# Optimization experiments

Measured on AMD Instinct MI355X. Metric: run time of the kernel, lower is better.

The kernel has to match this reference:

```python
import jax, jax.numpy as jnp
import numpy as np

B, S, D = 32, 512, 1024
H, HD = 16, 64          # num_heads, head_dim
K = 64                  # downsampling_k
NEG = -9e15             # -9000000000000000.0 in source


def setup_inputs() -> dict:
    key0 = jax.random.key(0)
    ks = jax.random.split(key0, 8)
    glorot = lambda k, shape, fan: jax.random.uniform(k, shape, jnp.float32,
                                                      -np.sqrt(6.0 / fan), np.sqrt(6.0 / fan))
    fan = D + H * HD  # glorot_uniform over (hidden, heads*head_dim)
    return {
        "query": jax.random.normal(ks[0], (B, S, D), jnp.float32),
        "key": jax.random.normal(ks[1], (B, S, D), jnp.float32),
        "value": jax.random.normal(ks[2], (B, S, D), jnp.float32),
        "query_kernel": glorot(ks[3], (D, H, HD), fan),
        "key_kernel": glorot(ks[4], (D, H, HD), fan),
        "value_kernel": glorot(ks[5], (D, H, HD), fan),
        "key_downsample_mat": (1.0 / K) * jax.random.normal(ks[6], (K, S), jnp.float32),
        "value_downsample_mat": (1.0 / K) * jax.random.normal(ks[7], (K, S), jnp.float32),
    }


def reference(query, key, value, query_kernel, key_kernel, value_kernel,
              key_downsample_mat, value_downsample_mat):
    # Linformer-style downsampling of K/V along the sequence axis: [B,S,D] -> [B,K,D]
    key_ds = jnp.einsum('ks,bsd->bkd', key_downsample_mat, key)
    val_ds = jnp.einsum('ks,bsd->bkd', value_downsample_mat, value)

    # Per-head projections
    q = jnp.einsum('bsd,dnh->bsnh', query, query_kernel)   # [B,S,H,HD]
    k = jnp.einsum('bkd,dnh->bknh', key_ds, key_kernel)    # [B,K,H,HD]
    v = jnp.einsum('bkd,dnh->bknh', val_ds, value_kernel)  # [B,K,H,HD]

    # Masked softmax attention over the downsampled key set
    scores = jnp.einsum('bqnh,bknh->bnqk', q, k)           # [B,H,S,K]
    # Source builds tril over [S, K_down] then slices first K cols (no-op here)
    mask = jnp.tril(jnp.ones((S, K), dtype=bool))          # [S,K], broadcasts over B,H
    scores = jnp.where(mask, scores, NEG)
    attn = jax.nn.softmax(scores, axis=-1)                 # dropout deterministic (train=False)

    a_v = jnp.einsum('bnqk,bknh->bqnh', attn, v)           # [B,S,H,HD]
    return a_v.reshape(B, S, H * HD)
```

## Files before the change

kernel.cpp:

```cpp
#include <hip/hip_runtime.h>
#include <stdint.h>

#define B_   32
#define S_   512
#define D_   1024
#define H_   16
#define HD_  64
#define KD_  64
#define NH_  1024

typedef __attribute__((ext_vector_type(8))) short short8;
typedef __attribute__((ext_vector_type(4))) float floatx4;

#define GAS __attribute__((address_space(1)))
#define LAS __attribute__((address_space(3)))

__device__ __forceinline__ ushort f2bf(float f) {
  uint32_t u = __float_as_uint(f);
  u = u + 0x7FFFu + ((u >> 16) & 1u);
  return (ushort)(u >> 16);
}

__device__ __forceinline__ float bf2f(ushort h) {
  return __uint_as_float(((uint32_t)h) << 16);
}

__device__ __forceinline__ void gload_lds16(const void* g, void* l) {
  __builtin_amdgcn_global_load_lds((const GAS uint32_t*)g, (LAS uint32_t*)l, 16, 0, 0);
}

#define BARRIER() asm volatile("s_barrier" ::: "memory")
#define WAITLGKM() asm volatile("s_waitcnt lgkmcnt(0)" ::: "memory")

__global__ __launch_bounds__(256) void cvt_split(const float* __restrict__ kdm,
                                                 const float* __restrict__ vdm,
                                                 ushort* __restrict__ hi,
                                                 ushort* __restrict__ lo) {
  int i = blockIdx.x * 256 + threadIdx.x;
  const float* src = (i < 8192) ? kdm : vdm;
  int j = i & 8191;
  float4 v = ((const float4*)src)[j];
  ushort4 h, l;
  h.x = f2bf(v.x); l.x = f2bf(v.x - bf2f(h.x));
  h.y = f2bf(v.y); l.y = f2bf(v.y - bf2f(h.y));
  h.z = f2bf(v.z); l.z = f2bf(v.z - bf2f(h.z));
  h.w = f2bf(v.w); l.w = f2bf(v.w - bf2f(h.w));
  ((ushort4*)hi)[i] = h;
  ((ushort4*)lo)[i] = l;
}

__global__ __launch_bounds__(256, 6) void pre_kv(
    const float* __restrict__ key, const float* __restrict__ value,
    const float* __restrict__ kkm, const float* __restrict__ vkm,
    const ushort* __restrict__ dsm_hi, const ushort* __restrict__ dsm_lo,
    ushort* __restrict__ kkT, ushort* __restrict__ vkT,
    ushort* __restrict__ outk, ushort* __restrict__ outv) {
  __shared__ __align__(16) char smem[17408];
  const int blk = blockIdx.x;
  const int tid = threadIdx.x;

  if (blk < 1024) {
    const int bz = (blk & 7) + ((blk >> 7) << 3);
    const int t  = (blk >> 3) & 15;
    const int z = bz >> 5, b = bz & 31;
    const int c0 = t * 64;
    const float* in = z ? value : key;
    ushort* out     = z ? outv : outk;
    const ushort* Ah = dsm_hi + (size_t)z * (KD_ * S_);
    const ushort* Al = dsm_lo + (size_t)z * (KD_ * S_);

    ushort* lAh = (ushort*)smem;
    ushort* lAl = (ushort*)(smem + 4096);
    uint*   lBh = (uint*)(smem + 8192);
    uint*   lBl = (uint*)(smem + 12800);

    const int lane = tid & 63, w = tid >> 6;
    const int lr = lane & 15, lg = lane >> 4;
    const int wn = w * 16;
    const int lam = tid & 15;
    const int d0 = lam * 4;
    const int sp = tid >> 4;
    const int swz = lam & 12;

    floatx4 acc[4];
#pragma unroll
    for (int m = 0; m < 4; ++m) acc[m] = (floatx4){0.f, 0.f, 0.f, 0.f};

    const float* pbase = in + (size_t)b * S_ * D_ + c0 + d0;
    float4 ra = *(const float4*)(pbase + (size_t)(sp * 2) * D_);
    float4 rb = *(const float4*)(pbase + (size_t)(sp * 2 + 1) * D_);

    for (int k0 = 0; k0 < S_; k0 += 32) {
      {
        size_t src = (size_t)(tid >> 2) * S_ + k0 + (size_t)(tid & 3) * 8;
        gload_lds16(Ah + src, lAh + w * 512);
        gload_lds16(Al + src, lAl + w * 512);
      }
      {
        int col = sp ^ swz;
        const float* pa = (const float*)&ra;
        const float* pb = (const float*)&rb;
#pragma unroll
        for (int i = 0; i < 4; ++i) {
          ushort h0 = f2bf(pa[i]);
          ushort l0 = f2bf(pa[i] - bf2f(h0));
          ushort h1 = f2bf(pb[i]);
          ushort l1 = f2bf(pb[i] - bf2f(h1));
          lBh[(d0 + i) * 18 + col] = (uint)h0 | ((uint)h1 << 16);
          lBl[(d0 + i) * 18 + col] = (uint)l0 | ((uint)l1 << 16);
        }
      }
      if (k0 + 32 < S_) {
        const float* pn = pbase + (size_t)(k0 + 32) * D_;
        ra = *(const float4*)(pn + (size_t)(sp * 2) * D_);
        rb = *(const float4*)(pn + (size_t)(sp * 2 + 1) * D_);
        asm volatile("s_waitcnt vmcnt(2)" ::: "memory");
      } else {
        asm volatile("s_waitcnt vmcnt(0)" ::: "memory");
      }
      WAITLGKM();
      BARRIER();
      short8 bh, bl;
      {
        int d = wn + lr;
        int off = d * 18 + ((lg * 4) ^ ((d >> 2) & 12));
        bh = *(const short8*)&lBh[off];
        bl = *(const short8*)&lBl[off];
      }
#pragma unroll
      for (int m = 0; m < 4; ++m) {
        int aoff = (m * 16 + lr) * 32 + lg * 8;
        short8 ah = *(const short8*)&lAh[aoff];
        short8 al = *(const short8*)&lAl[aoff];
        acc[m] = __builtin_amdgcn_mfma_f32_16x16x32_bf16(ah, bh, acc[m], 0, 0, 0);
        acc[m] = __builtin_amdgcn_mfma_f32_16x16x32_bf16(ah, bl, acc[m], 0, 0, 0);
        acc[m] = __builtin_amdgcn_mfma_f32_16x16x32_bf16(al, bh, acc[m], 0, 0, 0);
      }
      BARRIER();
    }
    size_t obase = (size_t)b * KD_ * D_;
#pragma unroll
    for (int m = 0; m < 4; ++m)
#pragma unroll
      for (int r = 0; r < 4; ++r)
        out[obase + (size_t)(m * 16 + lg * 4 + r) * D_ + c0 + wn + lr] =
            f2bf(acc[m][r]);

  } else {
    const int blk2 = blk - 1024;
    const int tz = blk2 >> 10;
    const int rem = blk2 & 1023;
    const int tyb = rem >> 5;
    const int txb = rem & 31;
    const float* in = tz == 0 ? kkm : vkm;
    ushort* outp    = tz == 0 ? kkT : vkT;
    float (*tile)[33] = (float(*)[33])smem;
    const int tx = tid & 31, ty = tid >> 5;
    int x = txb * 32 + tx;
    int y0 = tyb * 32;
#pragma unroll
    for (int j = 0; j < 4; ++j)
      tile[ty + j * 8][tx] = in[(size_t)(y0 + ty + j * 8) * 1024 + x];
    __syncthreads();
    int x2 = tyb * 32 + tx;
    int y2 = txb * 32;
#pragma unroll
    for (int j = 0; j < 4; ++j)
      outp[(size_t)(y2 + ty + j * 8) * 1024 + x2] = f2bf(tile[tx][ty + j * 8]);
  }
}

__global__ __launch_bounds__(256) void gemm_kv_q(
    const ushort* __restrict__ A,
    const ushort* __restrict__ Bt,
    const ushort* __restrict__ Bt2,
    ushort* __restrict__ C,
    ushort* __restrict__ vpT,
    const float* __restrict__ qk, ushort* __restrict__ qkT,
    const float* __restrict__ query, ushort* __restrict__ q_bf) {
  __shared__ __align__(16) char smem[16384];
  const int blk = blockIdx.x;
  const int tid = threadIdx.x;

  if (blk < 256) {
    ushort* lA = (ushort*)smem;
    ushort* lB = (ushort*)(smem + 8192);
    int xcd = blk & 7, slot = blk >> 3;
    int mt = xcd * 4 + (slot >> 3);
    int nt = slot & 7;
    int m0 = mt * 128, n0 = nt * 128;
    const ushort* Bsel = (mt >= 16) ? Bt2 : Bt;

    int lane = tid & 63, w = tid >> 6;
    int lr = lane & 15, lg = lane >> 4;
    int wm = (w >> 1) * 64, wn = (w & 1) * 64;
    floatx4 acc[4][4];
#pragma unroll
    for (int m = 0; m < 4; ++m)
#pragma unroll
      for (int n = 0; n < 4; ++n) acc[m][n] = (floatx4){0.f, 0.f, 0.f, 0.f};

    for (int k0 = 0; k0 < 1024; k0 += 32) {
#pragma unroll
      for (int i = 0; i < 2; ++i) {
        int c = i * 256 + w * 64 + lane;
        gload_lds16(A + ((size_t)(m0 + (c >> 2)) * 1024 + k0 + (c & 3) * 8),
                    &lA[(i * 256 + w * 64) * 8]);
        gload_lds16(Bsel + ((size_t)(n0 + (c >> 2)) * 1024 + k0 + (c & 3) * 8),
                    &lB[(i * 256 + w * 64) * 8]);
      }
      __syncthreads();
      short8 af[4], bfr[4];
#pragma unroll
      for (int m = 0; m < 4; ++m)
        af[m] = *(const short8*)&lA[(wm + m * 16 + lr) * 32 + lg * 8];
#pragma unroll
      for (int n = 0; n < 4; ++n)
        bfr[n] = *(const short8*)&lB[(wn + n * 16 + lr) * 32 + lg * 8];
#pragma unroll
      for (int m = 0; m < 4; ++m)
#pragma unroll
        for (int n = 0; n < 4; ++n)
          acc[m][n] = __builtin_amdgcn_mfma_f32_16x16x32_bf16(af[m], bfr[n], acc[m][n], 0, 0, 0);
      __syncthreads();
    }
    if (mt < 16) {
#pragma unroll
      for (int m = 0; m < 4; ++m)
#pragma unroll
        for (int n = 0; n < 4; ++n)
#pragma unroll
          for (int r = 0; r < 4; ++r)
            C[(size_t)(m0 + wm + m * 16 + lg * 4 + r) * 1024 + n0 + wn + n * 16 + lr] =
                f2bf(acc[m][n][r]);
    } else {
#pragma unroll
      for (int m = 0; m < 4; ++m)
#pragma unroll
        for (int n = 0; n < 4; ++n) {
          int rowV = m0 - 2048 + wm + m * 16 + lg * 4;
          int b = rowV >> 6, k = rowV & 63;
          int hd = n0 + wn + n * 16 + lr;
          ushort4 o;
          o.x = f2bf(acc[m][n][0]); o.y = f2bf(acc[m][n][1]);
          o.z = f2bf(acc[m][n][2]); o.w = f2bf(acc[m][n][3]);
          *(ushort4*)&vpT[(size_t)b * 65536 + (size_t)hd * 64 + k] = o;
        }
    }

  } else if (blk < 256 + 1024) {
    const int blk2 = blk - 256;
    const int tyb = blk2 >> 5;
    const int txb = blk2 & 31;
    float (*tile)[33] = (float(*)[33])smem;
    const int tx = tid & 31, ty = tid >> 5;
    int x = txb * 32 + tx;
    int y0 = tyb * 32;
#pragma unroll
    for (int j = 0; j < 4; ++j)
      tile[ty + j * 8][tx] = qk[(size_t)(y0 + ty + j * 8) * 1024 + x];
    __syncthreads();
    int x2 = tyb * 32 + tx;
    int y2 = txb * 32;
#pragma unroll
    for (int j = 0; j < 4; ++j)
      qkT[(size_t)(y2 + ty + j * 8) * 1024 + x2] = f2bf(tile[tx][ty + j * 8]);

  } else {
    const size_t base = (size_t)(blk - 1280) * 2048 + tid;
#pragma unroll
    for (int j = 0; j < 8; ++j) {
      size_t i = base + (size_t)j * 256;
      float4 v = ((const float4*)query)[i];
      ushort4 o;
      o.x = f2bf(v.x); o.y = f2bf(v.y); o.z = f2bf(v.z); o.w = f2bf(v.w);
      ((ushort4*)q_bf)[i] = o;
    }
  }
}

__global__ __launch_bounds__(512, 2) void gemm256_attn(
    const ushort* __restrict__ A, const ushort* __restrict__ Bt,
    const ushort* __restrict__ kp, const ushort* __restrict__ vpT,
    float* __restrict__ out) {
  extern __shared__ ushort lds[];
  ushort* ldsA = lds;
  ushort* ldsB = lds + 2 * 256 * 64;
  const int tid = threadIdx.x;
  const int w = tid >> 6, lane = tid & 63;
  const int lr = lane & 15, lg = lane >> 4;
  const int wm = w >> 2, wn = w & 3;
  const int bid = blockIdx.x;
  const int mt = (bid & 7) * 8 + ((bid >> 3) >> 2);
  const int nt = (bid >> 3) & 3;
  const int m0 = mt * 256, n0 = nt * 256;
  const int NT = 16;

  const int srow = tid >> 3;
  const int sslot = tid & 7;

  auto stageA = [&](int sl, int ch, int k0) {
    int rloc = ch * 64 + srow;
    int gs = sslot ^ (rloc & 7);
    gload_lds16(A + (size_t)(m0 + rloc) * 1024 + k0 + gs * 8,
                ldsA + sl * (256 * 64) + ch * (64 * 64) + w * 512);
  };
  auto stageB = [&](int sl, int ch, int k0) {
    int rloc = ch * 64 + srow;
    int gs = sslot ^ (rloc & 7);
    gload_lds16(Bt + (size_t)(n0 + rloc) * 1024 + k0 + gs * 8,
                ldsB + sl * (256 * 64) + ch * (64 * 64) + w * 512);
  };

  short8 af[4][2], bf[2][2];
  auto loadA = [&](int sl, int mh) {
#pragma unroll
    for (int i = 0; i < 4; ++i) {
      int row = wm * 128 + (mh * 4 + i) * 16 + lr;
#pragma unroll
      for (int kk = 0; kk < 2; ++kk) {
        int col = (((kk * 4 + lg) ^ (row & 7)) * 8);
        af[i][kk] = *(const short8*)&ldsA[sl * (256 * 64) + row * 64 + col];
      }
    }
  };
  auto loadB = [&](int sl, int nh) {
#pragma unroll
    for (int j = 0; j < 2; ++j) {
      int row = wn * 64 + (nh * 2 + j) * 16 + lr;
#pragma unroll
      for (int kk = 0; kk < 2; ++kk) {
        int col = (((kk * 4 + lg) ^ (row & 7)) * 8);
        bf[j][kk] = *(const short8*)&ldsB[sl * (256 * 64) + row * 64 + col];
      }
    }
  };

  floatx4 acc[8][4];
#pragma unroll
  for (int i = 0; i < 8; ++i)
#pragma unroll
    for (int j = 0; j < 4; ++j) acc[i][j] = (floatx4){0.f, 0.f, 0.f, 0.f};

  auto mma16 = [&](int mh, int nh) {
    __builtin_amdgcn_s_setprio(1);
#pragma unroll
    for (int i = 0; i < 4; ++i)
#pragma unroll
      for (int j = 0; j < 2; ++j)
#pragma unroll
        for (int kk = 0; kk < 2; ++kk)
          acc[mh * 4 + i][nh * 2 + j] = __builtin_amdgcn_mfma_f32_16x16x32_bf16(
              af[i][kk], bf[j][kk], acc[mh * 4 + i][nh * 2 + j], 0, 0, 0);
    __builtin_amdgcn_s_setprio(0);
  };

#pragma unroll
  for (int ch = 0; ch < 4; ++ch) { stageA(0, ch, 0); stageB(0, ch, 0); }

#pragma unroll 2
  for (int t = 0; t < NT; ++t) {
    const int s = t & 1, ns = s ^ 1;
    const int kn = (t + 1) << 6;
    const bool more = (t + 1 < NT);
    if (more) { stageA(ns, 0, kn); stageA(ns, 1, kn); }
    if (more) { asm volatile("s_waitcnt vmcnt(2)" ::: "memory"); }
    else      { asm volatile("s_waitcnt vmcnt(0)" ::: "memory"); }
    BARRIER();
    loadA(s, 0); loadB(s, 0);
    WAITLGKM();
    mma16(0, 0);
    BARRIER();
    loadB(s, 1);
    if (more) { stageB(ns, 0, kn); stageB(ns, 1, kn); }
    BARRIER();
    WAITLGKM();
    mma16(0, 1);
    BARRIER();
    loadA(s, 1);
    if (more) { stageA(ns, 2, kn); stageA(ns, 3, kn); }
    BARRIER();
    WAITLGKM();
    mma16(1, 1);
    BARRIER();
    loadB(s, 0);
    if (more) { stageB(ns, 2, kn); stageB(ns, 3, kn); }
    BARRIER();
    WAITLGKM();
    mma16(1, 0);
    BARRIER();
  }

  ushort* QP = lds + w * 4608;
  const int b = mt >> 1;
  const int hq = nt * 4 + wn;

#pragma unroll
  for (int half = 0; half < 2; ++half) {
    const int srow0 = (mt & 1) * 256 + wm * 128 + half * 64;
#pragma unroll
    for (int mi = 0; mi < 4; ++mi)
#pragma unroll
      for (int nj = 0; nj < 4; ++nj)
#pragma unroll
        for (int r = 0; r < 4; ++r)
          QP[(mi * 16 + lg * 4 + r) * 72 + nj * 16 + lr] =
              f2bf(acc[half * 4 + mi][nj][r]);
    WAITLGKM();
    __builtin_amdgcn_sched_barrier(0);
    floatx4 qacc[4][4];
#pragma unroll
    for (int m = 0; m < 4; ++m)
#pragma unroll
      for (int n = 0; n < 4; ++n) qacc[m][n] = (floatx4){0.f, 0.f, 0.f, 0.f};
#pragma unroll
    for (int kk = 0; kk < 2; ++kk) {
      short8 qa[4], kb[4];
#pragma unroll
      for (int m = 0; m < 4; ++m)
        qa[m] = *(const short8*)&QP[(m * 16 + lr) * 72 + kk * 32 + lg * 8];
#pragma unroll
      for (int n = 0; n < 4; ++n)
        kb[n] = *(const short8*)(kp + ((size_t)b * KD_ + n * 16 + lr) * 1024 +
                                 hq * HD_ + kk * 32 + lg * 8);
#pragma unroll
      for (int m = 0; m < 4; ++m)
#pragma unroll
        for (int n = 0; n < 4; ++n)
          qacc[m][n] = __builtin_amdgcn_mfma_f32_16x16x32_bf16(qa[m], kb[n], qacc[m][n], 0, 0, 0);
    }
#pragma unroll
    for (int m = 0; m < 4; ++m) {
#pragma unroll
      for (int r = 0; r < 4; ++r) {
        int srow2 = srow0 + m * 16 + lg * 4 + r;
        float vals[4];
        float mx = -1e30f;
#pragma unroll
        for (int n = 0; n < 4; ++n) {
          int col = n * 16 + lr;
          float val = qacc[m][n][r];
          val = (col <= srow2) ? val : -1e30f;
          vals[n] = val;
          mx = fmaxf(mx, val);
        }
        mx = fmaxf(mx, __shfl_xor(mx, 1));
        mx = fmaxf(mx, __shfl_xor(mx, 2));
        mx = fmaxf(mx, __shfl_xor(mx, 4));
        mx = fmaxf(mx, __shfl_xor(mx, 8));
        float sum = 0.f;
#pragma unroll
        for (int n = 0; n < 4; ++n) {
          float e = __expf(vals[n] - mx);
          vals[n] = e;
          sum += e;
        }
        sum += __shfl_xor(sum, 1);
        sum += __shfl_xor(sum, 2);
        sum += __shfl_xor(sum, 4);
        sum += __shfl_xor(sum, 8);
        float inv = 1.0f / sum;
#pragma unroll
        for (int n = 0; n < 4; ++n)
          QP[(m * 16 + lg * 4 + r) * 72 + n * 16 + lr] = f2bf(vals[n] * inv);
      }
    }
    WAITLGKM();
    __builtin_amdgcn_sched_barrier(0);
    floatx4 oacc[4][4];
#pragma unroll
    for (int m = 0; m < 4; ++m)
#pragma unroll
      for (int n = 0; n < 4; ++n) oacc[m][n] = (floatx4){0.f, 0.f, 0.f, 0.f};
#pragma unroll
    for (int kk = 0; kk < 2; ++kk) {
      short8 pa[4], vb[4];
#pragma unroll
      for (int m = 0; m < 4; ++m)
        pa[m] = *(const short8*)&QP[(m * 16 + lr) * 72 + kk * 32 + lg * 8];
#pragma unroll
      for (int n = 0; n < 4; ++n)
        vb[n] = *(const short8*)(vpT + (size_t)b * 65536 +
                                 (size_t)(hq * HD_ + n * 16 + lr) * 64 +
                                 kk * 32 + lg * 8);
#pragma unroll
      for (int m = 0; m < 4; ++m)
#pragma unroll
        for (int n = 0; n < 4; ++n)
          oacc[m][n] = __builtin_amdgcn_mfma_f32_16x16x32_bf16(pa[m], vb[n], oacc[m][n], 0, 0, 0);
    }
#pragma unroll
    for (int m = 0; m < 4; ++m)
#pragma unroll
      for (int n = 0; n < 4; ++n)
#pragma unroll
        for (int r = 0; r < 4; ++r)
          out[((size_t)b * S_ + srow0 + m * 16 + lg * 4 + r) * 1024 +
              hq * HD_ + n * 16 + lr] = oacc[m][n][r];
  }
}

extern "C" void kernel_launch(void* const* d_in, const int* in_sizes, int n_in,
                              void* d_out, int out_size, void* d_ws, size_t ws_size,
                              hipStream_t stream) {
  const float* query = (const float*)d_in[0];
  const float* key   = (const float*)d_in[1];
  const float* value = (const float*)d_in[2];
  const float* qk    = (const float*)d_in[3];
  const float* kk    = (const float*)d_in[4];
  const float* vk    = (const float*)d_in[5];
  const float* kdm   = (const float*)d_in[6];
  const float* vdm   = (const float*)d_in[7];
  float* out = (float*)d_out;

  char* ws = (char*)d_ws;
  if (ws_size < (90ull << 20)) return;
  ushort* q_bf   = (ushort*)(ws);
  ushort* qkT    = (ushort*)(ws + (33ull << 20));
  ushort* kkT    = (ushort*)(ws + (35ull << 20));
  ushort* vkT    = (ushort*)(ws + (37ull << 20));
  ushort* kds    = (ushort*)(ws + (39ull << 20));
  ushort* vds    = (ushort*)(ws + (43ull << 20));
  ushort* k_proj = (ushort*)(ws + (79ull << 20));
  ushort* v_projT= (ushort*)(ws + (83ull << 20));
  ushort* dsm_hi = (ushort*)(ws + (87ull << 20));
  ushort* dsm_lo = (ushort*)(ws + (87ull << 20) + (128ull << 10));

  hipFuncSetAttribute((const void*)gemm256_attn,
                      hipFuncAttributeMaxDynamicSharedMemorySize, 131072);

  cvt_split<<<64, 256, 0, stream>>>(kdm, vdm, dsm_hi, dsm_lo);
  pre_kv<<<1024 + 2048, 256, 0, stream>>>(
      key, value, kk, vk, dsm_hi, dsm_lo, kkT, vkT, kds, vds);
  gemm_kv_q<<<256 + 1024 + 2048, 256, 0, stream>>>(
      kds, kkT, vkT, k_proj, v_projT, qk, qkT, query, q_bf);
  gemm256_attn<<<256, 512, 131072, stream>>>(q_bf, qkT, k_proj, v_projT, out);
}
```

Baseline: 129.4 us.

## Fuse fp32-to-bf16 query conversion into the Q-projection GEMM A-operand staging

After: 166.8 us. 28.9% more time.

```diff
diff --git a/kernel.cpp b/kernel.cpp
--- a/kernel.cpp
+++ b/kernel.cpp
@@ -176,8 +176,7 @@
     const ushort* __restrict__ Bt2,
     ushort* __restrict__ C,
     ushort* __restrict__ vpT,
-    const float* __restrict__ qk, ushort* __restrict__ qkT,
-    const float* __restrict__ query, ushort* __restrict__ q_bf) {
+    const float* __restrict__ qk, ushort* __restrict__ qkT) {
   __shared__ __align__(16) char smem[16384];
   const int blk = blockIdx.x;
   const int tid = threadIdx.x;
@@ -248,7 +247,7 @@
         }
     }
 
-  } else if (blk < 256 + 1024) {
+  } else {
     const int blk2 = blk - 256;
     const int tyb = blk2 >> 5;
     const int txb = blk2 & 31;
@@ -265,22 +264,11 @@
 #pragma unroll
     for (int j = 0; j < 4; ++j)
       qkT[(size_t)(y2 + ty + j * 8) * 1024 + x2] = f2bf(tile[tx][ty + j * 8]);
-
-  } else {
-    const size_t base = (size_t)(blk - 1280) * 2048 + tid;
-#pragma unroll
-    for (int j = 0; j < 8; ++j) {
-      size_t i = base + (size_t)j * 256;
-      float4 v = ((const float4*)query)[i];
-      ushort4 o;
-      o.x = f2bf(v.x); o.y = f2bf(v.y); o.z = f2bf(v.z); o.w = f2bf(v.w);
-      ((ushort4*)q_bf)[i] = o;
-    }
   }
 }
 
 __global__ __launch_bounds__(512, 2) void gemm256_attn(
-    const ushort* __restrict__ A, const ushort* __restrict__ Bt,
+    const float* __restrict__ qf, const ushort* __restrict__ Bt,
     const ushort* __restrict__ kp, const ushort* __restrict__ vpT,
     float* __restrict__ out) {
   extern __shared__ ushort lds[];
@@ -299,11 +287,29 @@
   const int srow = tid >> 3;
   const int sslot = tid & 7;
 
-  auto stageA = [&](int sl, int ch, int k0) {
-    int rloc = ch * 64 + srow;
-    int gs = sslot ^ (rloc & 7);
-    gload_lds16(A + (size_t)(m0 + rloc) * 1024 + k0 + gs * 8,
-                ldsA + sl * (256 * 64) + ch * (64 * 64) + w * 512);
+  float4 aq[8];
+  auto loadAq = [&](int k0) {
+#pragma unroll
+    for (int ch = 0; ch < 4; ++ch) {
+      int rloc = ch * 64 + srow;
+      int gs = sslot ^ (rloc & 7);
+      const float* src = qf + (size_t)(m0 + rloc) * 1024 + k0 + gs * 8;
+      aq[ch * 2]     = *(const float4*)src;
+      aq[ch * 2 + 1] = *(const float4*)(src + 4);
+    }
+  };
+  auto writeAq = [&](int sl) {
+#pragma unroll
+    for (int ch = 0; ch < 4; ++ch) {
+      const float* p0 = (const float*)&aq[ch * 2];
+      const float* p1 = (const float*)&aq[ch * 2 + 1];
+      ushort4 o0, o1;
+      o0.x = f2bf(p0[0]); o0.y = f2bf(p0[1]); o0.z = f2bf(p0[2]); o0.w = f2bf(p0[3]);
+      o1.x = f2bf(p1[0]); o1.y = f2bf(p1[1]); o1.z = f2bf(p1[2]); o1.w = f2bf(p1[3]);
+      ushort* dst = ldsA + sl * (256 * 64) + ch * (64 * 64) + w * 512 + lane * 8;
+      *(ushort4*)dst = o0;
+      *(ushort4*)(dst + 4) = o1;
+    }
   };
   auto stageB = [&](int sl, int ch, int k0) {
     int rloc = ch * 64 + srow;
@@ -355,16 +361,19 @@
     __builtin_amdgcn_s_setprio(0);
   };
 
-#pragma unroll
-  for (int ch = 0; ch < 4; ++ch) { stageA(0, ch, 0); stageB(0, ch, 0); }
+  loadAq(0);
+#pragma unroll
+  for (int ch = 0; ch < 4; ++ch) stageB(0, ch, 0);
+  asm volatile("s_waitcnt vmcnt(4)" ::: "memory");
+  writeAq(0);
+  WAITLGKM();
 
 #pragma unroll 2
   for (int t = 0; t < NT; ++t) {
     const int s = t & 1, ns = s ^ 1;
     const int kn = (t + 1) << 6;
     const bool more = (t + 1 < NT);
-    if (more) { stageA(ns, 0, kn); stageA(ns, 1, kn); }
-    if (more) { asm volatile("s_waitcnt vmcnt(2)" ::: "memory"); }
+    if (more) { loadAq(kn); asm volatile("s_waitcnt vmcnt(8)" ::: "memory"); }
     else      { asm volatile("s_waitcnt vmcnt(0)" ::: "memory"); }
     BARRIER();
     loadA(s, 0); loadB(s, 0);
@@ -378,7 +387,7 @@
     mma16(0, 1);
     BARRIER();
     loadA(s, 1);
-    if (more) { stageA(ns, 2, kn); stageA(ns, 3, kn); }
+    if (more) { asm volatile("s_waitcnt vmcnt(2)" ::: "memory"); writeAq(ns); }
     BARRIER();
     WAITLGKM();
     mma16(1, 1);
@@ -515,7 +524,6 @@
 
   char* ws = (char*)d_ws;
   if (ws_size < (90ull << 20)) return;
-  ushort* q_bf   = (ushort*)(ws);
   ushort* qkT    = (ushort*)(ws + (33ull << 20));
   ushort* kkT    = (ushort*)(ws + (35ull << 20));
   ushort* vkT    = (ushort*)(ws + (37ull << 20));
@@ -532,7 +540,7 @@
   cvt_split<<<64, 256, 0, stream>>>(kdm, vdm, dsm_hi, dsm_lo);
   pre_kv<<<1024 + 2048, 256, 0, stream>>>(
       key, value, kk, vk, dsm_hi, dsm_lo, kkT, vkT, kds, vds);
-  gemm_kv_q<<<256 + 1024 + 2048, 256, 0, stream>>>(
-      kds, kkT, vkT, k_proj, v_projT, qk, qkT, query, q_bf);
-  gemm256_attn<<<256, 512, 131072, stream>>>(q_bf, qkT, k_proj, v_projT, out);
-}
+  gemm_kv_q<<<256 + 1024, 256, 0, stream>>>(
+      kds, kkT, vkT, k_proj, v_projT, qk, qkT);
+  gemm256_attn<<<256, 512, 131072, stream>>>(query, qkT, k_proj, v_projT, out);
+}
```
